# Performance work log

Hardware: AMD Instinct MI355X
Metric: run time of the kernel (lower is better)

The kernel has to match this reference:

```python
import jax, jax.numpy as jnp
import numpy as np

C = 256
NH = 4  # attention heads
G = 8   # groupnorm groups
EPS = 1e-5


def group_norm(x, weight, bias):
    B, Cc, H, W = x.shape
    xg = x.reshape(B, G, Cc // G, H, W)
    mean = xg.mean(axis=(2, 3, 4), keepdims=True)
    var = xg.var(axis=(2, 3, 4), keepdims=True)
    xg = (xg - mean) * jax.lax.rsqrt(var + EPS)
    xn = xg.reshape(B, Cc, H, W)
    return xn * weight[None, :, None, None] + bias[None, :, None, None]


def setup_inputs() -> dict:
    key = jax.random.key(0)
    ks = jax.random.split(key, 7)
    B, H, W = 16, 32, 32
    x = jax.random.normal(ks[0], (B, C, H, W), dtype=jnp.float32)
    n_weight = jnp.ones((C,), dtype=jnp.float32)
    n_bias = jnp.zeros((C,), dtype=jnp.float32)
    qkv_w = jax.random.normal(ks[1], (3 * C, C), dtype=jnp.float32) * (C ** -0.5)
    qkv_b = jnp.zeros((3 * C,), dtype=jnp.float32)
    p_w = jax.random.normal(ks[2], (C, C), dtype=jnp.float32) * (C ** -0.5)
    p_b = jnp.zeros((C,), dtype=jnp.float32)
    return {"x": x, "n_weight": n_weight, "n_bias": n_bias,
            "qkv_w": qkv_w, "qkv_b": qkv_b, "p_w": p_w, "p_b": p_b}


def reference(x, n_weight, n_bias, qkv_w, qkv_b, p_w, p_b):
    B, Cc, H, W = x.shape
    N = H * W
    dh = Cc // NH
    sc = dh ** -0.5
    xn = group_norm(x, n_weight, n_bias)  # [B,C,H,W]
    xn_flat = xn.reshape(B, Cc, N)
    # 1x1 conv == channel matmul
    qkv = jnp.einsum('oc,bcn->bon', qkv_w, xn_flat) + qkv_b[None, :, None]
    qkv = qkv.reshape(B, 3, NH, dh, N)
    q, k, v = qkv[:, 0], qkv[:, 1], qkv[:, 2]  # [B,h,dh,N]
    a = jax.nn.softmax(jnp.einsum('bhci,bhcj->bhij', q, k) * sc, axis=-1)
    o = jnp.einsum('bhij,bhcj->bhci', a, v).reshape(B, Cc, N)
    proj = jnp.einsum('oc,bcn->bon', p_w, o) + p_b[None, :, None]
    return x + proj.reshape(B, Cc, H, W)
```

## Files before the change

kernel.cpp:

```cpp
#include <hip/hip_runtime.h>
#include <math.h>

typedef unsigned short ushort;
typedef unsigned int uint;
typedef __attribute__((ext_vector_type(8))) short bf16x8;
typedef __attribute__((ext_vector_type(4))) float f32x4;
typedef __attribute__((ext_vector_type(16))) float f32x16;
typedef __attribute__((ext_vector_type(2))) unsigned uint2v;

constexpr int Bc  = 16;
constexpr float EPSc = 1e-5f;
constexpr float QSC  = 0.18033688f;

__device__ __forceinline__ uint cvt2(float a, float b) {
    uint r;
    asm("v_cvt_pk_bf16_f32 %0, %1, %2" : "=v"(r) : "v"(a), "v"(b));
    return r;
}
__device__ __forceinline__ ushort f2bf_fast(float f) {
    uint r;
    asm("v_cvt_pk_bf16_f32 %0, %1, %2" : "=v"(r) : "v"(f), "v"(f));
    return (ushort)r;
}
__device__ __forceinline__ uint2v plswap(uint a, uint b) {
#if __has_builtin(__builtin_amdgcn_permlane32_swap)
    return __builtin_amdgcn_permlane32_swap(a, b, false, false);
#else
    asm volatile("v_permlane32_swap_b32 %0, %1" : "+v"(a), "+v"(b));
    uint2v r; r.x = a; r.y = b; return r;
#endif
}
#if __has_builtin(__builtin_amdgcn_exp2f)
#define EXP2F(x) __builtin_amdgcn_exp2f(x)
#else
#define EXP2F(x) __expf((x) * 0.69314718f)
#endif
__device__ __forceinline__ void gl_lds16(const ushort* g, ushort* l) {
    __builtin_amdgcn_global_load_lds(
        (const __attribute__((address_space(1))) void*)g,
        (__attribute__((address_space(3))) void*)l, 16, 0, 0);
}

__global__ __launch_bounds__(1024, 4) void norm_k(
    const float* __restrict__ x, const float* __restrict__ nw,
    const float* __restrict__ nb, const float* __restrict__ qkvw,
    const float* __restrict__ pw, ushort* __restrict__ xt,
    ushort* __restrict__ wqb, ushort* __restrict__ pwb) {
    int blk = blockIdx.x;
    int t = threadIdx.x;
    if (blk < 128) {
        int b = blk >> 3, g = blk & 7;
        const float* xs = x + ((size_t)(b * 8 + g)) * 32768;
        const float4* p4 = (const float4*)xs;
        float s = 0.f, s2 = 0.f;
#pragma unroll
        for (int i = 0; i < 8; ++i) {
            float4 v = p4[t + i * 1024];
            s += (v.x + v.y) + (v.z + v.w);
            s2 += (v.x * v.x + v.y * v.y) + (v.z * v.z + v.w * v.w);
        }
#pragma unroll
        for (int off = 1; off < 64; off <<= 1) {
            s += __shfl_xor(s, off);
            s2 += __shfl_xor(s2, off);
        }
        __shared__ float rs[16], rq[16], bc[2];
        int wv = t >> 6, lane = t & 63;
        if (lane == 0) { rs[wv] = s; rq[wv] = s2; }
        __syncthreads();
        if (t == 0) {
            float ts = 0.f, tq = 0.f;
#pragma unroll
            for (int i = 0; i < 16; ++i) { ts += rs[i]; tq += rq[i]; }
            float mean = ts * (1.f / 32768.f);
            float var  = tq * (1.f / 32768.f) - mean * mean;
            bc[0] = mean; bc[1] = rsqrtf(var + EPSc);
        }
        __syncthreads();
        float mean = bc[0], inv = bc[1];
        int n = (t & 255) * 4;
        int cg = (t >> 8) * 8;
        uint pk[4][4];
#pragma unroll
        for (int cp = 0; cp < 4; ++cp) {
            int c0 = cg + cp * 2;
            float w0 = inv * nw[g * 32 + c0];
            float b0 = nb[g * 32 + c0] - mean * w0;
            float w1 = inv * nw[g * 32 + c0 + 1];
            float b1 = nb[g * 32 + c0 + 1] - mean * w1;
            float4 v0 = *(const float4*)&xs[(size_t)c0 * 1024 + n];
            float4 v1 = *(const float4*)&xs[(size_t)(c0 + 1) * 1024 + n];
            pk[0][cp] = cvt2(v0.x * w0 + b0, v1.x * w1 + b1);
            pk[1][cp] = cvt2(v0.y * w0 + b0, v1.y * w1 + b1);
            pk[2][cp] = cvt2(v0.z * w0 + b0, v1.z * w1 + b1);
            pk[3][cp] = cvt2(v0.w * w0 + b0, v1.w * w1 + b1);
        }
#pragma unroll
        for (int k = 0; k < 4; ++k) {
            uint4 u; u.x = pk[k][0]; u.y = pk[k][1]; u.z = pk[k][2]; u.w = pk[k][3];
            *(uint4*)&xt[((size_t)(b * 1024 + n + k)) * 256 + g * 32 + cg] = u;
        }
    } else {
        int idx = ((blk - 128) * 1024 + t) * 4;
        if (idx < 196608) {
            int row = idx >> 8;
            float sc = (row < 256) ? QSC : 1.f;
            float4 v = *(const float4*)&qkvw[idx];
            uint2 u; u.x = cvt2(v.x * sc, v.y * sc); u.y = cvt2(v.z * sc, v.w * sc);
            *(uint2*)&wqb[idx] = u;
        } else {
            int j = idx - 196608;
            float4 v = *(const float4*)&pw[j];
            uint2 u; u.x = cvt2(v.x, v.y); u.y = cvt2(v.z, v.w);
            *(uint2*)&pwb[j] = u;
        }
    }
}

__global__ __launch_bounds__(256, 2) void qkv_gemm_k(
    const ushort* __restrict__ wq, const ushort* __restrict__ xt,
    const float* __restrict__ wb, ushort* __restrict__ qkT,
    ushort* __restrict__ vbuf) {
    int b = blockIdx.z, cy = blockIdx.y, sx = blockIdx.x;
    __shared__ ushort SB[2][2][128 * 64];
    int t = threadIdx.x, lane = t & 63, w = t >> 6;
    int quad = lane >> 4, l15 = lane & 15;
    int wm = w >> 1, wn = w & 1;
    const ushort* wrow = wq + (size_t)cy * 128 * 256;
    const ushort* xrow = xt + ((size_t)b * 1024 + sx * 128) * 256;
    bool tpath = (cy < 4);
    int r0 = t >> 3;
    int cs = (t & 7) ^ (r0 & 7);
    int dst = t * 8;
#pragma unroll
    for (int ps = 0; ps < 4; ++ps) {
        int r = r0 + ps * 32;
        gl_lds16(&wrow[(size_t)r * 256 + cs * 8], &SB[0][0][ps * 2048 + dst]);
        gl_lds16(&xrow[(size_t)r * 256 + cs * 8], &SB[0][1][ps * 2048 + dst]);
    }
    __syncthreads();
    int s0 = quad ^ (l15 & 7);
    f32x4 acc[4][4] = {};
    int cur = 0;
    for (int ki = 0; ki < 4; ++ki) {
        if (ki < 3) {
            int k0 = (ki + 1) * 64, nx = cur ^ 1;
#pragma unroll
            for (int ps = 0; ps < 4; ++ps) {
                int r = r0 + ps * 32;
                gl_lds16(&wrow[(size_t)r * 256 + k0 + cs * 8], &SB[nx][0][ps * 2048 + dst]);
                gl_lds16(&xrow[(size_t)r * 256 + k0 + cs * 8], &SB[nx][1][ps * 2048 + dst]);
            }
        }
        const ushort* Wc = SB[cur][0];
        const ushort* Xc = SB[cur][1];
        const ushort* Am = tpath ? Xc : Wc;
        const ushort* Bn = tpath ? Wc : Xc;
#pragma unroll
        for (int kk = 0; kk < 2; ++kk) {
            int sl = s0 ^ (kk * 4);
            bf16x8 fa[4], fb[4];
#pragma unroll
            for (int mi = 0; mi < 4; ++mi)
                fa[mi] = *(const bf16x8*)&Am[(wm * 64 + mi * 16 + l15) * 64 + sl * 8];
#pragma unroll
            for (int ni = 0; ni < 4; ++ni)
                fb[ni] = *(const bf16x8*)&Bn[(wn * 64 + ni * 16 + l15) * 64 + sl * 8];
#pragma unroll
            for (int mi = 0; mi < 4; ++mi)
#pragma unroll
                for (int ni = 0; ni < 4; ++ni)
                    acc[mi][ni] = __builtin_amdgcn_mfma_f32_16x16x32_bf16(
                        fa[mi], fb[ni], acc[mi][ni], 0, 0, 0);
        }
        __syncthreads();
        cur ^= 1;
    }
    __syncthreads();
    ushort* Tw = ((ushort*)SB) + w * (64 * 72);
    float bsc = (tpath && cy < 2) ? QSC : 1.f;
    if (tpath) {
#pragma unroll
        for (int ni = 0; ni < 4; ++ni) {
            float bias = wb[cy * 128 + wn * 64 + ni * 16 + l15] * bsc;
#pragma unroll
            for (int mi = 0; mi < 4; ++mi)
#pragma unroll
                for (int rr = 0; rr < 4; ++rr)
                    Tw[(mi * 16 + quad * 4 + rr) * 72 + ni * 16 + l15] =
                        f2bf_fast(acc[mi][ni][rr] + bias);
        }
    } else {
#pragma unroll
        for (int mi = 0; mi < 4; ++mi)
#pragma unroll
            for (int rr = 0; rr < 4; ++rr) {
                float bias = wb[cy * 128 + wm * 64 + mi * 16 + quad * 4 + rr];
#pragma unroll
                for (int ni = 0; ni < 4; ++ni)
                    Tw[(mi * 16 + quad * 4 + rr) * 72 + ni * 16 + l15] =
                        f2bf_fast(acc[mi][ni][rr] + bias);
            }
    }
    __asm__ __volatile__("" ::: "memory");
    int row8 = lane >> 3, ch = lane & 7;
#pragma unroll
    for (int p = 0; p < 8; ++p) {
        int row = p * 8 + row8;
        uint4 u = *(const uint4*)&Tw[row * 72 + ch * 8];
        if (tpath) {
            int sp = sx * 128 + wm * 64 + row;
            *(uint4*)&qkT[((size_t)b * 1024 + sp) * 512 + cy * 128 + wn * 64 + ch * 8] = u;
        } else {
            int chanloc = (cy - 4) * 128 + wm * 64 + row;
            *(uint4*)&vbuf[((size_t)b * 256 + chanloc) * 1024 + sx * 128 + wn * 64 + ch * 8] = u;
        }
    }
}

__global__ __launch_bounds__(256, 2) void attn_k(
    const ushort* __restrict__ qkT, const ushort* __restrict__ vbuf,
    ushort* __restrict__ ot) {
    int bh = blockIdx.x;
    int i0 = blockIdx.y * 128;
    int b = bh >> 2, h = bh & 3;
    const ushort* qTb = qkT + (size_t)b * 1024 * 512 + h * 64;
    const ushort* kTb = qTb + 256;
    const ushort* vb  = vbuf + ((size_t)(b * 256 + h * 64)) * 1024;
    __shared__ ushort SM[32768];
    ushort* Ks0 = SM;
    ushort* Vs0 = SM + 16384;
    int t = threadIdx.x, lane = t & 63, wv = t >> 6;
    int l31 = lane & 31, hf = lane >> 5;
    int rk = t >> 3, pk = t & 7;
    int rv = t >> 4, pv = t & 15;
#pragma unroll
    for (int seg = 0; seg < 4; ++seg) {
        int krow = seg * 32 + rk;
        int kc = pk ^ (krow & 7);
        gl_lds16(&kTb[(size_t)krow * 512 + kc * 8], &Ks0[seg * 2048 + t * 8]);
        int vrow = seg * 16 + rv;
        int vc = pv ^ (vrow & 7);
        gl_lds16(&vb[(size_t)vrow * 1024 + vc * 8], &Vs0[seg * 2048 + t * 8]);
    }
    bf16x8 qf[4];
#pragma unroll
    for (int ks = 0; ks < 4; ++ks)
        qf[ks] = *(const bf16x8*)
            &qTb[(size_t)(i0 + wv * 32 + l31) * 512 + ks * 16 + hf * 8];
    __syncthreads();
    f32x16 oT0 = {}, oT1 = {};
    float lsum = 0.f;
    int cur = 0;
    for (int j0 = 0; j0 < 1024; j0 += 128) {
        ushort* Kc = Ks0 + cur * 8192;
        ushort* Vc = Vs0 + cur * 8192;
        if (j0 < 896) {
            int nx = cur ^ 1;
            ushort* Kn = Ks0 + nx * 8192;
            ushort* Vn = Vs0 + nx * 8192;
#pragma unroll
            for (int seg = 0; seg < 4; ++seg) {
                int krow = seg * 32 + rk;
                int kc = pk ^ (krow & 7);
                gl_lds16(&kTb[(size_t)(j0 + 128 + krow) * 512 + kc * 8], &Kn[seg * 2048 + t * 8]);
                int vrow = seg * 16 + rv;
                int vc = pv ^ (vrow & 7);
                gl_lds16(&vb[(size_t)vrow * 1024 + j0 + 128 + vc * 8], &Vn[seg * 2048 + t * 8]);
            }
        }
#pragma unroll
        for (int jb = 0; jb < 4; ++jb) {
            f32x16 s = {};
            __builtin_amdgcn_s_setprio(1);
#pragma unroll
            for (int ks = 0; ks < 4; ++ks) {
                int row = jb * 32 + l31;
                int c = (2 * ks + hf) ^ (row & 7);
                bf16x8 ak = *(const bf16x8*)&Kc[row * 64 + c * 8];
                s = __builtin_amdgcn_mfma_f32_32x32x16_bf16(ak, qf[ks], s, 0, 0, 0);
            }
            __builtin_amdgcn_s_setprio(0);
            uint w0[4], w1[4];
#pragma unroll
            for (int q = 0; q < 4; ++q) {
                float e0 = EXP2F(s[q * 4 + 0]), e1 = EXP2F(s[q * 4 + 1]);
                float e2 = EXP2F(s[q * 4 + 2]), e3 = EXP2F(s[q * 4 + 3]);
                lsum += (e0 + e1) + (e2 + e3);
                w0[q] = cvt2(e0, e1);
                w1[q] = cvt2(e2, e3);
            }
            bf16x8 pf[2];
#pragma unroll
            for (int s2 = 0; s2 < 2; ++s2) {
                uint2v ra = plswap(w0[2 * s2], w0[2 * s2 + 1]);
                uint2v rb = plswap(w1[2 * s2], w1[2 * s2 + 1]);
                uint4 u; u.x = ra.x; u.y = rb.x; u.z = ra.y; u.w = rb.y;
                bf16x8 v; __builtin_memcpy(&v, &u, 16);
                pf[s2] = v;
            }
            __builtin_amdgcn_s_setprio(1);
#pragma unroll
            for (int s2 = 0; s2 < 2; ++s2) {
#pragma unroll
                for (int db = 0; db < 2; ++db) {
                    int row = db * 32 + l31;
                    int c = (jb * 4 + s2 * 2 + hf) ^ (row & 7);
                    bf16x8 av = *(const bf16x8*)&Vc[row * 128 + c * 8];
                    if (db == 0)
                        oT0 = __builtin_amdgcn_mfma_f32_32x32x16_bf16(av, pf[s2], oT0, 0, 0, 0);
                    else
                        oT1 = __builtin_amdgcn_mfma_f32_32x32x16_bf16(av, pf[s2], oT1, 0, 0, 0);
                }
            }
            __builtin_amdgcn_s_setprio(0);
        }
        __syncthreads();
        cur ^= 1;
    }
    lsum += __shfl_xor(lsum, 32);
    float linv = 1.f / lsum;
    uint* Os = (uint*)SM + wv * (32 * 33);
#pragma unroll
    for (int db = 0; db < 2; ++db) {
        f32x16 ov = (db == 0) ? oT0 : oT1;
#pragma unroll
        for (int q = 0; q < 4; ++q) {
            uint wa  = cvt2(ov[q * 4 + 0] * linv, ov[q * 4 + 1] * linv);
            uint wb2 = cvt2(ov[q * 4 + 2] * linv, ov[q * 4 + 3] * linv);
            int base = l31 * 33 + db * 16 + q * 4 + 2 * hf;
            Os[base]     = wa;
            Os[base + 1] = wb2;
        }
    }
    __asm__ __volatile__("" ::: "memory");
#pragma unroll
    for (int rr = 0; rr < 4; ++rr) {
        int irow = (lane >> 3) + rr * 8;
        const uint* rp = &Os[irow * 33 + (lane & 7) * 4];
        uint4 u; u.x = rp[0]; u.y = rp[1]; u.z = rp[2]; u.w = rp[3];
        *(uint4*)&ot[((size_t)b * 1024 + i0 + wv * 32 + irow) * 256 + h * 64 + (lane & 7) * 8] = u;
    }
}

__global__ __launch_bounds__(256, 3) void proj_k(
    const ushort* __restrict__ pwb, const ushort* __restrict__ ot,
    const float* __restrict__ pb, const float* __restrict__ x,
    float* __restrict__ out) {
    int b = blockIdx.z, cy = blockIdx.y, sx = blockIdx.x;
    __shared__ ushort SB[2][12288];
    int t = threadIdx.x, lane = t & 63, w = t >> 6;
    int quad = lane >> 4, l15 = lane & 15;
    int wm = w >> 1, wn = w & 1;
    const ushort* wrow = pwb + (size_t)cy * 128 * 256;
    const ushort* xrow = ot + ((size_t)b * 1024 + sx * 64) * 256;
    int r0 = t >> 3;
    int cs = (t & 7) ^ (r0 & 7);
    int dst = t * 8;
#pragma unroll
    for (int ps = 0; ps < 4; ++ps)
        gl_lds16(&wrow[(size_t)(r0 + ps * 32) * 256 + cs * 8], &SB[0][ps * 2048 + dst]);
#pragma unroll
    for (int ps = 0; ps < 2; ++ps)
        gl_lds16(&xrow[(size_t)(r0 + ps * 32) * 256 + cs * 8], &SB[0][8192 + ps * 2048 + dst]);
    __syncthreads();
    int p0 = quad ^ (l15 & 7);
    f32x4 acc[4][2] = {};
    int cur = 0;
    for (int ki = 0; ki < 4; ++ki) {
        if (ki < 3) {
            int k0 = (ki + 1) * 64, nx = cur ^ 1;
#pragma unroll
            for (int ps = 0; ps < 4; ++ps)
                gl_lds16(&wrow[(size_t)(r0 + ps * 32) * 256 + k0 + cs * 8], &SB[nx][ps * 2048 + dst]);
#pragma unroll
            for (int ps = 0; ps < 2; ++ps)
                gl_lds16(&xrow[(size_t)(r0 + ps * 32) * 256 + k0 + cs * 8], &SB[nx][8192 + ps * 2048 + dst]);
        }
        const ushort* Wc = &SB[cur][0];
        const ushort* Xc = &SB[cur][8192];
#pragma unroll
        for (int kk = 0; kk < 2; ++kk) {
            int sl = p0 ^ (kk * 4);
            bf16x8 fa[4], fb[2];
#pragma unroll
            for (int mi = 0; mi < 4; ++mi)
                fa[mi] = *(const bf16x8*)&Wc[(wm * 64 + mi * 16 + l15) * 64 + sl * 8];
#pragma unroll
            for (int ni = 0; ni < 2; ++ni)
                fb[ni] = *(const bf16x8*)&Xc[(wn * 32 + ni * 16 + l15) * 64 + sl * 8];
#pragma unroll
            for (int mi = 0; mi < 4; ++mi)
#pragma unroll
                for (int ni = 0; ni < 2; ++ni)
                    acc[mi][ni] = __builtin_amdgcn_mfma_f32_16x16x32_bf16(
                        fa[mi], fb[ni], acc[mi][ni], 0, 0, 0);
        }
        __syncthreads();
        cur ^= 1;
    }
#pragma unroll
    for (int mi = 0; mi < 4; ++mi)
#pragma unroll
        for (int rr = 0; rr < 4; ++rr) {
            int chan = cy * 128 + wm * 64 + mi * 16 + quad * 4 + rr;
            float bias = pb[chan];
#pragma unroll
            for (int ni = 0; ni < 2; ++ni) {
                int sp = sx * 64 + wn * 32 + ni * 16 + l15;
                size_t o = ((size_t)(b * 256 + chan)) * 1024 + sp;
                float xr = __builtin_nontemporal_load(&x[o]);
                __builtin_nontemporal_store(acc[mi][ni][rr] + bias + xr, &out[o]);
            }
        }
}

extern "C" void kernel_launch(void* const* d_in, const int* in_sizes, int n_in,
                              void* d_out, int out_size, void* d_ws, size_t ws_size,
                              hipStream_t stream) {
    const float* x    = (const float*)d_in[0];
    const float* nw   = (const float*)d_in[1];
    const float* nb   = (const float*)d_in[2];
    const float* qkvw = (const float*)d_in[3];
    const float* qkvb = (const float*)d_in[4];
    const float* pw   = (const float*)d_in[5];
    const float* pb   = (const float*)d_in[6];
    float* out = (float*)d_out;

    ushort* base = (ushort*)d_ws;
    ushort* xt   = base;
    ushort* wqb  = xt + (size_t)16 * 1024 * 256;
    ushort* pwb  = wqb + 768 * 256;
    ushort* qkT  = pwb + 256 * 256;
    ushort* vbuf = qkT + (size_t)16 * 1024 * 512;
    ushort* ot   = xt;

    norm_k<<<dim3(192), dim3(1024), 0, stream>>>(x, nw, nb, qkvw, pw, xt, wqb, pwb);
    qkv_gemm_k<<<dim3(8, 6, Bc), dim3(256), 0, stream>>>(wqb, xt, qkvb, qkT, vbuf);
    attn_k<<<dim3(64, 8), dim3(256), 0, stream>>>(qkT, vbuf, ot);
    proj_k<<<dim3(16, 2, Bc), dim3(256), 0, stream>>>(pwb, ot, pb, x, out);
}
```

Baseline: 125.3 us.

## Halve QKV GEMM K-tile to cut LDS and raise occupancy to three blocks

```diff
diff --git a/kernel.cpp b/kernel.cpp
--- a/kernel.cpp
+++ b/kernel.cpp
@@ -117,67 +117,70 @@
     }
 }
 
-__global__ __launch_bounds__(256, 2) void qkv_gemm_k(
+__global__ __launch_bounds__(256, 3) void qkv_gemm_k(
     const ushort* __restrict__ wq, const ushort* __restrict__ xt,
     const float* __restrict__ wb, ushort* __restrict__ qkT,
     ushort* __restrict__ vbuf) {
     int b = blockIdx.z, cy = blockIdx.y, sx = blockIdx.x;
-    __shared__ ushort SB[2][2][128 * 64];
+    __shared__ ushort SM[18432];
     int t = threadIdx.x, lane = t & 63, w = t >> 6;
     int quad = lane >> 4, l15 = lane & 15;
     int wm = w >> 1, wn = w & 1;
     const ushort* wrow = wq + (size_t)cy * 128 * 256;
     const ushort* xrow = xt + ((size_t)b * 1024 + sx * 128) * 256;
     bool tpath = (cy < 4);
-    int r0 = t >> 3;
-    int cs = (t & 7) ^ (r0 & 7);
-    int dst = t * 8;
-#pragma unroll
-    for (int ps = 0; ps < 4; ++ps) {
-        int r = r0 + ps * 32;
-        gl_lds16(&wrow[(size_t)r * 256 + cs * 8], &SB[0][0][ps * 2048 + dst]);
-        gl_lds16(&xrow[(size_t)r * 256 + cs * 8], &SB[0][1][ps * 2048 + dst]);
-    }
+    int R0 = t >> 3, cc_s = t & 7;
+    auto stage = [&](const ushort* mat, ushort* dstbuf, int k0) {
+#pragma unroll
+        for (int ps = 0; ps < 2; ++ps) {
+            int R = R0 + ps * 32;
+            int cc0 = cc_s ^ (R & 7);
+            int gr = 2 * R + (cc0 >> 2);
+            int gc = (cc0 & 3) * 8;
+            gl_lds16(&mat[(size_t)gr * 256 + k0 + gc], &dstbuf[(ps * 256 + t) * 8]);
+        }
+    };
+    stage(wrow, SM, 0);
+    stage(xrow, SM + 4096, 0);
     __syncthreads();
-    int s0 = quad ^ (l15 & 7);
     f32x4 acc[4][4] = {};
     int cur = 0;
-    for (int ki = 0; ki < 4; ++ki) {
-        if (ki < 3) {
-            int k0 = (ki + 1) * 64, nx = cur ^ 1;
-#pragma unroll
-            for (int ps = 0; ps < 4; ++ps) {
-                int r = r0 + ps * 32;
-                gl_lds16(&wrow[(size_t)r * 256 + k0 + cs * 8], &SB[nx][0][ps * 2048 + dst]);
-                gl_lds16(&xrow[(size_t)r * 256 + k0 + cs * 8], &SB[nx][1][ps * 2048 + dst]);
-            }
-        }
-        const ushort* Wc = SB[cur][0];
-        const ushort* Xc = SB[cur][1];
+    for (int ki = 0; ki < 8; ++ki) {
+        if (ki < 7) {
+            int k0 = (ki + 1) * 32, nx = cur ^ 1;
+            stage(wrow, SM + nx * 8192, k0);
+            stage(xrow, SM + nx * 8192 + 4096, k0);
+        }
+        const ushort* Wc = SM + cur * 8192;
+        const ushort* Xc = SM + cur * 8192 + 4096;
         const ushort* Am = tpath ? Xc : Wc;
         const ushort* Bn = tpath ? Wc : Xc;
-#pragma unroll
-        for (int kk = 0; kk < 2; ++kk) {
-            int sl = s0 ^ (kk * 4);
-            bf16x8 fa[4], fb[4];
-#pragma unroll
-            for (int mi = 0; mi < 4; ++mi)
-                fa[mi] = *(const bf16x8*)&Am[(wm * 64 + mi * 16 + l15) * 64 + sl * 8];
+        bf16x8 fa[4], fb[4];
+#pragma unroll
+        for (int mi = 0; mi < 4; ++mi) {
+            int r = wm * 64 + mi * 16 + l15;
+            int R = r >> 1;
+            int cc = ((r & 1) * 4 + quad) ^ (R & 7);
+            fa[mi] = *(const bf16x8*)&Am[R * 64 + cc * 8];
+        }
+#pragma unroll
+        for (int ni = 0; ni < 4; ++ni) {
+            int r = wn * 64 + ni * 16 + l15;
+            int R = r >> 1;
+            int cc = ((r & 1) * 4 + quad) ^ (R & 7);
+            fb[ni] = *(const bf16x8*)&Bn[R * 64 + cc * 8];
+        }
+#pragma unroll
+        for (int mi = 0; mi < 4; ++mi)
 #pragma unroll
             for (int ni = 0; ni < 4; ++ni)
-                fb[ni] = *(const bf16x8*)&Bn[(wn * 64 + ni * 16 + l15) * 64 + sl * 8];
-#pragma unroll
-            for (int mi = 0; mi < 4; ++mi)
-#pragma unroll
-                for (int ni = 0; ni < 4; ++ni)
-                    acc[mi][ni] = __builtin_amdgcn_mfma_f32_16x16x32_bf16(
-                        fa[mi], fb[ni], acc[mi][ni], 0, 0, 0);
-        }
+                acc[mi][ni] = __builtin_amdgcn_mfma_f32_16x16x32_bf16(
+                    fa[mi], fb[ni], acc[mi][ni], 0, 0, 0);
         __syncthreads();
         cur ^= 1;
     }
     __syncthreads();
-    ushort* Tw = ((ushort*)SB) + w * (64 * 72);
+    ushort* Tw = SM + w * 4608;
     float bsc = (tpath && cy < 2) ? QSC : 1.f;
     if (tpath) {
 #pragma unroll
```

Result: no change. 125.1 us (-0.2%).
